# Kernel tuning notes

Hardware: AMD Instinct MI355X
Metric: run time of the kernel (lower is better)

The kernel has to match this reference:

```python
import jax, jax.numpy as jnp
import numpy as np

B, T, C, H = 4, 2048, 1024, 16
D = C // H  # head_dim = 64

def setup_inputs() -> dict:
    key = jax.random.key(0)
    ks = jax.random.split(key, 5)
    scale = 1.0 / np.sqrt(C)
    return {
        "x": jax.random.normal(ks[0], (B, T, C), dtype=jnp.float32),
        "Wq": jax.random.normal(ks[1], (C, C), dtype=jnp.float32) * scale,
        "Wk": jax.random.normal(ks[2], (C, C), dtype=jnp.float32) * scale,
        "Wv": jax.random.normal(ks[3], (C, C), dtype=jnp.float32) * scale,
        "Wo": jax.random.normal(ks[4], (C, C), dtype=jnp.float32) * scale,
        "bo": jnp.zeros((C,), dtype=jnp.float32),
    }

def reference(x, Wq, Wk, Wv, Wo, bo):
    Bx, Tx, Cx = x.shape
    # projections -> [B, H, T, D]
    def split_heads(y):
        return y.reshape(Bx, Tx, H, D).transpose(0, 2, 1, 3)
    Q = split_heads(x @ Wq)
    K = split_heads(x @ Wk)
    V = split_heads(x @ Wv)
    # scaled dot-product with causal mask: [B, H, T, T]
    scores = jnp.einsum('bhqd,bhkd->bhqk', Q, K) / jnp.sqrt(jnp.asarray(D, x.dtype))
    causal = jnp.tril(jnp.ones((Tx, Tx), dtype=bool))
    scores = jnp.where(causal, scores, -jnp.inf)
    weights = jax.nn.softmax(scores, axis=-1)
    attn = jnp.einsum('bhqk,bhkd->bhqd', weights, V)  # [B, H, T, D]
    out = attn.transpose(0, 2, 1, 3).reshape(Bx, Tx, Cx)
    return out @ Wo + bo
```

## Files before the change

### kernel.cpp

```cpp
#include <hip/hip_runtime.h>
#include <hip/hip_bf16.h>
#include <cmath>

typedef __bf16 bf16;
typedef __bf16 bf16x8 __attribute__((ext_vector_type(8)));
typedef __bf16 bf16x4v __attribute__((ext_vector_type(4)));
typedef float f32x4 __attribute__((ext_vector_type(4)));

#define B_ 4
#define T_ 2048
#define C_ 1024
#define H_ 16
#define D_ 64
#define BT_ 8192
#define LOG2E 1.4426950408889634f

__device__ __forceinline__ void async_cp16(const void* g, void* l) {
  __builtin_amdgcn_global_load_lds(
      (__attribute__((address_space(1))) void*)g,
      (__attribute__((address_space(3))) void*)l, 16, 0, 0);
}

__device__ __forceinline__ f32x4 mfma16(bf16x8 a, bf16x8 b, f32x4 c) {
  return __builtin_amdgcn_mfma_f32_16x16x32_bf16(a, b, c, 0, 0, 0);
}

__global__ __launch_bounds__(256) void cast_x_kernel(
    const float* __restrict__ in, bf16* __restrict__ out, int n4) {
  int i = blockIdx.x * 256 + threadIdx.x;
  if (i >= n4) return;
  float4 v = ((const float4*)in)[i];
  bf16x4v o = {(bf16)v.x, (bf16)v.y, (bf16)v.z, (bf16)v.w};
  ((bf16x4v*)out)[i] = o;
}

__global__ __launch_bounds__(256) void transpose_cast_kernel(
    const float* __restrict__ W, bf16* __restrict__ Wt) {
  __shared__ float tile[32][33];
  const int x = threadIdx.x, y = threadIdx.y;
  const int n0 = blockIdx.x * 32, k0 = blockIdx.y * 32;
#pragma unroll
  for (int j = 0; j < 32; j += 8)
    tile[y + j][x] = W[(size_t)(k0 + y + j) * C_ + n0 + x];
  __syncthreads();
#pragma unroll
  for (int j = 0; j < 32; j += 8)
    Wt[(size_t)(n0 + y + j) * C_ + k0 + x] = (bf16)tile[x][y + j];
}

template <int F32OUT>
__global__ __launch_bounds__(256, 2) void gemm_bt_kernel(
    const bf16* __restrict__ A, const bf16* __restrict__ Bt,
    void* __restrict__ Cv, const float* __restrict__ bias,
    int M, int N, int K) {
  __shared__ __align__(16) bf16 As[128 * 32];
  __shared__ __align__(16) bf16 Bs[128 * 32];
  const int t = threadIdx.x;
  const int lane = t & 63;
  const int wave = t >> 6;
  const int quad = lane >> 4;
  const int l15 = lane & 15;
  const int m0 = blockIdx.y * 128;
  const int n0 = blockIdx.x * 128;
  const int wm = (wave >> 1) * 64;
  const int wn = (wave & 1) * 64;
  const int srow = t >> 2;
  const int scol = (t & 3) * 8;

  const bf16* Ag = A + (size_t)(m0 + srow) * K + scol;
  const bf16* Bg = Bt + (size_t)(n0 + srow) * K + scol;
  bf16* Asd = &As[srow * 32 + scol];
  bf16* Asd2 = &As[(srow + 64) * 32 + scol];
  bf16* Bsd = &Bs[srow * 32 + scol];
  bf16* Bsd2 = &Bs[(srow + 64) * 32 + scol];

  f32x4 acc[4][4] = {};

  for (int kt = 0; kt < K; kt += 32) {
    async_cp16(Ag + kt, Asd);
    async_cp16(Ag + kt + (size_t)64 * K, Asd2);
    async_cp16(Bg + kt, Bsd);
    async_cp16(Bg + kt + (size_t)64 * K, Bsd2);
    __syncthreads();
    bf16x8 af[4], bfr[4];
#pragma unroll
    for (int i = 0; i < 4; i++)
      af[i] = *(const bf16x8*)&As[(wm + i * 16 + l15) * 32 + quad * 8];
#pragma unroll
    for (int j = 0; j < 4; j++)
      bfr[j] = *(const bf16x8*)&Bs[(wn + j * 16 + l15) * 32 + quad * 8];
#pragma unroll
    for (int i = 0; i < 4; i++)
#pragma unroll
      for (int j = 0; j < 4; j++)
        acc[i][j] = mfma16(af[i], bfr[j], acc[i][j]);
    __syncthreads();
  }

#pragma unroll
  for (int i = 0; i < 4; i++) {
    const int gr = m0 + wm + i * 16 + quad * 4;
#pragma unroll
    for (int j = 0; j < 4; j++) {
      const int gc = n0 + wn + j * 16 + l15;
      const float bv = F32OUT ? bias[gc] : 0.0f;
#pragma unroll
      for (int r = 0; r < 4; r++) {
        const float v = acc[i][j][r] + bv;
        if (F32OUT)
          ((float*)Cv)[(size_t)(gr + r) * N + gc] = v;
        else
          ((bf16*)Cv)[(size_t)(gr + r) * N + gc] = (bf16)v;
      }
    }
  }
}

__global__ __launch_bounds__(256, 3) void flash_attn_kernel(
    const bf16* __restrict__ qk, const bf16* __restrict__ vt,
    bf16* __restrict__ attn) {
  __shared__ __align__(16) char smem[49152];
  bf16* Ks = (bf16*)smem;
  bf16* Vs = (bf16*)(smem + 16384);
  bf16* Ps = (bf16*)(smem + 32768);

  const int t = threadIdx.x;
  const int lane = t & 63;
  const int wave = t >> 6;
  const int quad = lane >> 4;
  const int l15 = lane & 15;
  const int l7 = l15 & 7;
  const int bx = blockIdx.x;
  const int qt = 15 - (bx >> 6);
  const int bh = bx & 63;
  const int b = bh >> 4;
  const int h = bh & 15;

  const bf16* Qg = qk + (size_t)b * T_ * 2048 + h * 64;
  const bf16* Kg = qk + (size_t)b * T_ * 2048 + 1024 + h * 64;
  const bf16* Vg = vt + (size_t)h * 64 * BT_ + b * T_;

  bf16x8 qf[2][2];
  const int qrow0 = qt * 128 + wave * 32;
#pragma unroll
  for (int mt = 0; mt < 2; mt++)
#pragma unroll
    for (int ks = 0; ks < 2; ks++) {
      bf16x8 v = *(const bf16x8*)(Qg + (size_t)(qrow0 + mt * 16 + l15) * 2048 +
                                  ks * 32 + quad * 8);
#pragma unroll
      for (int j = 0; j < 8; j++) v[j] = (bf16)((float)v[j] * 0.125f);
      qf[mt][ks] = v;
    }

  f32x4 o_acc[4][2] = {};
  f32x4 l4[2] = {};

  const int krofs = lane >> 3;
  const int kck = (lane & 7) ^ krofs;
  const int vdofs = lane >> 4;
  const int vpc = lane & 15;
  const int pswz = (l15 & 3) << 2;

  for (int jt = 0; jt <= qt; jt++) {
    const int k0 = jt * 128;

    {
      const bf16* gK = Kg + (size_t)(k0 + wave * 32 + krofs) * 2048 + kck * 8;
      bf16* lK = Ks + wave * 2048 + lane * 8;
#pragma unroll
      for (int i = 0; i < 4; i++)
        async_cp16(gK + (size_t)(i * 8) * 2048, lK + i * 512);
    }
    {
#pragma unroll
      for (int i = 0; i < 4; i++) {
        const int d = wave * 16 + i * 4 + vdofs;
        const int cv = vpc ^ (d & 7);
        async_cp16(Vg + (size_t)d * BT_ + k0 + cv * 8,
                   Vs + (wave * 16 + i * 4) * 128 + lane * 8);
      }
    }
    __syncthreads();

    bf16x4v p[2][8];
    const bool diag = (jt == qt);
#pragma unroll
    for (int kt = 0; kt < 8; kt++) {
      const bf16x8 kf0 =
          *(const bf16x8*)&Ks[(kt * 16 + l15) * 64 + (quad ^ l7) * 8];
      const bf16x8 kf1 =
          *(const bf16x8*)&Ks[(kt * 16 + l15) * 64 + ((4 + quad) ^ l7) * 8];
#pragma unroll
      for (int mt = 0; mt < 2; mt++) {
        f32x4 s = mfma16(kf0, qf[mt][0], f32x4{0.f, 0.f, 0.f, 0.f});
        s = mfma16(kf1, qf[mt][1], s);
        if (diag) {
          const int q_loc = wave * 32 + mt * 16 + l15;
#pragma unroll
          for (int i = 0; i < 4; i++)
            if (kt * 16 + quad * 4 + i > q_loc) s[i] = -INFINITY;
        }
        f32x4 e;
#pragma unroll
        for (int i = 0; i < 4; i++)
          e[i] = __builtin_amdgcn_exp2f(s[i] * LOG2E);
        l4[mt] += e;
        p[mt][kt] = bf16x4v{(bf16)e[0], (bf16)e[1], (bf16)e[2], (bf16)e[3]};
      }
    }

#pragma unroll
    for (int hh = 0; hh < 2; hh++) {
#pragma unroll
      for (int mt = 0; mt < 2; mt++) {
        const int row = wave * 32 + mt * 16 + l15;
#pragma unroll
        for (int kt = 0; kt < 4; kt++) {
          const int c = kt * 4 + quad;
          *(bf16x4v*)&Ps[row * 64 + (c ^ pswz) * 4] = p[mt][hh * 4 + kt];
        }
      }
#pragma unroll
      for (int ks2 = 0; ks2 < 2; ks2++) {
        bf16x8 pa[2], vb[4];
#pragma unroll
        for (int mt = 0; mt < 2; mt++) {
          const int row = wave * 32 + mt * 16 + l15;
          const int c0 = ks2 * 8 + quad * 2;
          pa[mt] = *(const bf16x8*)&Ps[row * 64 + (c0 ^ pswz) * 4];
        }
#pragma unroll
        for (int dt = 0; dt < 4; dt++) {
          const int vc = (hh * 8 + ks2 * 4 + quad) ^ l7;
          vb[dt] = *(const bf16x8*)&Vs[(dt * 16 + l15) * 128 + vc * 8];
        }
#pragma unroll
        for (int dt = 0; dt < 4; dt++)
#pragma unroll
          for (int mt = 0; mt < 2; mt++)
            o_acc[dt][mt] = mfma16(vb[dt], pa[mt], o_acc[dt][mt]);
      }
    }
    __syncthreads();
  }

  float inv[2];
#pragma unroll
  for (int mt = 0; mt < 2; mt++) {
    float l = l4[mt][0] + l4[mt][1] + l4[mt][2] + l4[mt][3];
    l += __shfl_xor(l, 16, 64);
    l += __shfl_xor(l, 32, 64);
    inv[mt] = 1.0f / l;
  }
#pragma unroll
  for (int dt = 0; dt < 4; dt++)
#pragma unroll
    for (int mt = 0; mt < 2; mt++) {
      const int q = qt * 128 + wave * 32 + mt * 16 + l15;
      bf16x4v o = {(bf16)(o_acc[dt][mt][0] * inv[mt]),
                   (bf16)(o_acc[dt][mt][1] * inv[mt]),
                   (bf16)(o_acc[dt][mt][2] * inv[mt]),
                   (bf16)(o_acc[dt][mt][3] * inv[mt])};
      *(bf16x4v*)(attn + (size_t)(b * T_ + q) * 1024 + h * 64 + dt * 16 +
                  quad * 4) = o;
    }
}

extern "C" void kernel_launch(void* const* d_in, const int* in_sizes, int n_in,
                              void* d_out, int out_size, void* d_ws,
                              size_t ws_size, hipStream_t stream) {
  const float* x = (const float*)d_in[0];
  const float* Wq = (const float*)d_in[1];
  const float* Wk = (const float*)d_in[2];
  const float* Wv = (const float*)d_in[3];
  const float* Wo = (const float*)d_in[4];
  const float* bo = (const float*)d_in[5];
  float* out = (float*)d_out;

  char* ws = (char*)d_ws;
  bf16* xb = (bf16*)(ws);
  bf16* qkb = (bf16*)(ws + 16777216);
  bf16* vtb = (bf16*)(ws + 50331648);
  bf16* attn = (bf16*)(ws + 67108864);
  bf16* wqkvT = (bf16*)(ws + 83886080);
  bf16* woT = (bf16*)(ws + 90177536);

  cast_x_kernel<<<8192, 256, 0, stream>>>(x, xb, 2097152);

  dim3 tb(32, 8), tg(32, 32);
  transpose_cast_kernel<<<tg, tb, 0, stream>>>(Wq, wqkvT);
  transpose_cast_kernel<<<tg, tb, 0, stream>>>(Wk, wqkvT + 1024 * 1024);
  transpose_cast_kernel<<<tg, tb, 0, stream>>>(Wv, wqkvT + 2 * 1024 * 1024);
  transpose_cast_kernel<<<tg, tb, 0, stream>>>(Wo, woT);

  gemm_bt_kernel<0><<<dim3(16, 64), 256, 0, stream>>>(
      xb, wqkvT, (void*)qkb, nullptr, 8192, 2048, 1024);

  gemm_bt_kernel<0><<<dim3(64, 8), 256, 0, stream>>>(
      wqkvT + 2 * 1024 * 1024, xb, (void*)vtb, nullptr, 1024, 8192, 1024);

  flash_attn_kernel<<<1024, 256, 0, stream>>>(qkb, vtb, attn);

  gemm_bt_kernel<1><<<dim3(8, 64), 256, 0, stream>>>(
      attn, woT, (void*)out, bo, 8192, 1024, 1024);
}
```

Baseline: 270.9 us.

## Double-buffer attention KV tiles, widen GEMM K-tile, merge weight transposes

The flash attention loop now works on 64-key tiles with two LDS buffers, issuing the async load of the next tile before computing the current one. This is meant to hide global-load latency and removes the trailing barrier. The GEMM now uses a 64-wide K tile with an XOR-swizzled LDS layout and occupancy hint 3, halving barrier count per K. The four weight transpose-cast launches are merged into one 3D-grid launch. Risks: more LDS per block could limit occupancy, and smaller attention tiles double the number of barriers per key range.

New measurement: 239.8 us. 11.5% less time.

```diff
diff --git a/kernel.cpp b/kernel.cpp
--- a/kernel.cpp
+++ b/kernel.cpp
@@ -34,9 +34,14 @@
   ((bf16x4v*)out)[i] = o;
 }
 
-__global__ __launch_bounds__(256) void transpose_cast_kernel(
-    const float* __restrict__ W, bf16* __restrict__ Wt) {
+__global__ __launch_bounds__(256) void transpose_cast4_kernel(
+    const float* __restrict__ Wq, const float* __restrict__ Wk,
+    const float* __restrict__ Wv, const float* __restrict__ Wo,
+    bf16* __restrict__ dst) {
   __shared__ float tile[32][33];
+  const int z = blockIdx.z;
+  const float* W = (z == 0) ? Wq : (z == 1) ? Wk : (z == 2) ? Wv : Wo;
+  bf16* Wt = dst + (size_t)z * 1048576;
   const int x = threadIdx.x, y = threadIdx.y;
   const int n0 = blockIdx.x * 32, k0 = blockIdx.y * 32;
 #pragma unroll
@@ -49,51 +54,56 @@
 }
 
 template <int F32OUT>
-__global__ __launch_bounds__(256, 2) void gemm_bt_kernel(
+__global__ __launch_bounds__(256, 3) void gemm_bt_kernel(
     const bf16* __restrict__ A, const bf16* __restrict__ Bt,
     void* __restrict__ Cv, const float* __restrict__ bias,
     int M, int N, int K) {
-  __shared__ __align__(16) bf16 As[128 * 32];
-  __shared__ __align__(16) bf16 Bs[128 * 32];
+  __shared__ __align__(16) bf16 As[128 * 64];
+  __shared__ __align__(16) bf16 Bs[128 * 64];
   const int t = threadIdx.x;
   const int lane = t & 63;
   const int wave = t >> 6;
   const int quad = lane >> 4;
   const int l15 = lane & 15;
+  const int l7 = l15 & 7;
   const int m0 = blockIdx.y * 128;
   const int n0 = blockIdx.x * 128;
   const int wm = (wave >> 1) * 64;
   const int wn = (wave & 1) * 64;
-  const int srow = t >> 2;
-  const int scol = (t & 3) * 8;
-
-  const bf16* Ag = A + (size_t)(m0 + srow) * K + scol;
-  const bf16* Bg = Bt + (size_t)(n0 + srow) * K + scol;
-  bf16* Asd = &As[srow * 32 + scol];
-  bf16* Asd2 = &As[(srow + 64) * 32 + scol];
-  bf16* Bsd = &Bs[srow * 32 + scol];
-  bf16* Bsd2 = &Bs[(srow + 64) * 32 + scol];
+
+  const int sr8 = lane >> 3;
+  const int sc = (lane & 7) ^ sr8;
+  const bf16* Ag = A + (size_t)(m0 + wave * 32 + sr8) * K + sc * 8;
+  const bf16* Bg = Bt + (size_t)(n0 + wave * 32 + sr8) * K + sc * 8;
+  bf16* Ad = As + wave * 2048 + lane * 8;
+  bf16* Bd = Bs + wave * 2048 + lane * 8;
 
   f32x4 acc[4][4] = {};
 
-  for (int kt = 0; kt < K; kt += 32) {
-    async_cp16(Ag + kt, Asd);
-    async_cp16(Ag + kt + (size_t)64 * K, Asd2);
-    async_cp16(Bg + kt, Bsd);
-    async_cp16(Bg + kt + (size_t)64 * K, Bsd2);
+  for (int kt = 0; kt < K; kt += 64) {
+#pragma unroll
+    for (int i = 0; i < 4; i++) {
+      async_cp16(Ag + kt + (size_t)(i * 8) * K, Ad + i * 512);
+      async_cp16(Bg + kt + (size_t)(i * 8) * K, Bd + i * 512);
+    }
     __syncthreads();
-    bf16x8 af[4], bfr[4];
-#pragma unroll
-    for (int i = 0; i < 4; i++)
-      af[i] = *(const bf16x8*)&As[(wm + i * 16 + l15) * 32 + quad * 8];
-#pragma unroll
-    for (int j = 0; j < 4; j++)
-      bfr[j] = *(const bf16x8*)&Bs[(wn + j * 16 + l15) * 32 + quad * 8];
-#pragma unroll
-    for (int i = 0; i < 4; i++)
+#pragma unroll
+    for (int ks = 0; ks < 2; ks++) {
+      bf16x8 af[4], bfr[4];
+#pragma unroll
+      for (int i = 0; i < 4; i++)
+        af[i] = *(const bf16x8*)&As[(wm + i * 16 + l15) * 64 +
+                                    (((ks * 4 + quad) ^ l7) * 8)];
 #pragma unroll
       for (int j = 0; j < 4; j++)
-        acc[i][j] = mfma16(af[i], bfr[j], acc[i][j]);
+        bfr[j] = *(const bf16x8*)&Bs[(wn + j * 16 + l15) * 64 +
+                                     (((ks * 4 + quad) ^ l7) * 8)];
+#pragma unroll
+      for (int i = 0; i < 4; i++)
+#pragma unroll
+        for (int j = 0; j < 4; j++)
+          acc[i][j] = mfma16(af[i], bfr[j], acc[i][j]);
+    }
     __syncthreads();
   }
 
@@ -119,9 +129,9 @@
 __global__ __launch_bounds__(256, 3) void flash_attn_kernel(
     const bf16* __restrict__ qk, const bf16* __restrict__ vt,
     bf16* __restrict__ attn) {
-  __shared__ __align__(16) char smem[49152];
-  bf16* Ks = (bf16*)smem;
-  bf16* Vs = (bf16*)(smem + 16384);
+  __shared__ __align__(16) char smem[51200];
+  bf16* KsB = (bf16*)smem;
+  bf16* VsB = (bf16*)(smem + 16384);
   bf16* Ps = (bf16*)(smem + 32768);
 
   const int t = threadIdx.x;
@@ -156,93 +166,83 @@
   f32x4 o_acc[4][2] = {};
   f32x4 l4[2] = {};
 
-  const int krofs = lane >> 3;
-  const int kck = (lane & 7) ^ krofs;
-  const int vdofs = lane >> 4;
-  const int vpc = lane & 15;
-  const int pswz = (l15 & 3) << 2;
-
-  for (int jt = 0; jt <= qt; jt++) {
-    const int k0 = jt * 128;
-
-    {
-      const bf16* gK = Kg + (size_t)(k0 + wave * 32 + krofs) * 2048 + kck * 8;
-      bf16* lK = Ks + wave * 2048 + lane * 8;
-#pragma unroll
-      for (int i = 0; i < 4; i++)
-        async_cp16(gK + (size_t)(i * 8) * 2048, lK + i * 512);
-    }
-    {
-#pragma unroll
-      for (int i = 0; i < 4; i++) {
-        const int d = wave * 16 + i * 4 + vdofs;
-        const int cv = vpc ^ (d & 7);
-        async_cp16(Vg + (size_t)d * BT_ + k0 + cv * 8,
-                   Vs + (wave * 16 + i * 4) * 128 + lane * 8);
-      }
-    }
+  const int sr8 = lane >> 3;
+  const int sc = (lane & 7) ^ sr8;
+
+  auto stage = [&](int j64, int buf) {
+    const int k0 = j64 * 64;
+    bf16* KL = KsB + buf * 4096 + wave * 1024 + lane * 8;
+    const bf16* KG = Kg + (size_t)(k0 + wave * 16 + sr8) * 2048 + sc * 8;
+    async_cp16(KG, KL);
+    async_cp16(KG + (size_t)8 * 2048, KL + 512);
+    bf16* VL = VsB + buf * 4096 + wave * 1024 + lane * 8;
+    const bf16* VG = Vg + (size_t)(wave * 16 + sr8) * BT_ + k0 + sc * 8;
+    async_cp16(VG, VL);
+    async_cp16(VG + (size_t)8 * BT_, VL + 512);
+  };
+
+  const int S = 2 * qt + 2;
+  stage(0, 0);
+
+  for (int s = 0; s < S; s++) {
     __syncthreads();
-
-    bf16x4v p[2][8];
-    const bool diag = (jt == qt);
-#pragma unroll
-    for (int kt = 0; kt < 8; kt++) {
+    if (s + 1 < S) stage(s + 1, (s + 1) & 1);
+    const bf16* Kb = KsB + (s & 1) * 4096;
+    const bf16* Vb = VsB + (s & 1) * 4096;
+    const int k0 = s * 64;
+    const bool diag = (s >= 2 * qt);
+
+    bf16x4v p[2][4];
+#pragma unroll
+    for (int kt = 0; kt < 4; kt++) {
       const bf16x8 kf0 =
-          *(const bf16x8*)&Ks[(kt * 16 + l15) * 64 + (quad ^ l7) * 8];
+          *(const bf16x8*)&Kb[(kt * 16 + l15) * 64 + ((quad ^ l7) * 8)];
       const bf16x8 kf1 =
-          *(const bf16x8*)&Ks[(kt * 16 + l15) * 64 + ((4 + quad) ^ l7) * 8];
+          *(const bf16x8*)&Kb[(kt * 16 + l15) * 64 + (((4 + quad) ^ l7) * 8)];
 #pragma unroll
       for (int mt = 0; mt < 2; mt++) {
-        f32x4 s = mfma16(kf0, qf[mt][0], f32x4{0.f, 0.f, 0.f, 0.f});
-        s = mfma16(kf1, qf[mt][1], s);
+        f32x4 sv = mfma16(kf0, qf[mt][0], f32x4{0.f, 0.f, 0.f, 0.f});
+        sv = mfma16(kf1, qf[mt][1], sv);
         if (diag) {
-          const int q_loc = wave * 32 + mt * 16 + l15;
+          const int qg = qt * 128 + wave * 32 + mt * 16 + l15;
 #pragma unroll
           for (int i = 0; i < 4; i++)
-            if (kt * 16 + quad * 4 + i > q_loc) s[i] = -INFINITY;
+            if (k0 + kt * 16 + quad * 4 + i > qg) sv[i] = -INFINITY;
         }
         f32x4 e;
 #pragma unroll
         for (int i = 0; i < 4; i++)
-          e[i] = __builtin_amdgcn_exp2f(s[i] * LOG2E);
+          e[i] = __builtin_amdgcn_exp2f(sv[i] * LOG2E);
         l4[mt] += e;
         p[mt][kt] = bf16x4v{(bf16)e[0], (bf16)e[1], (bf16)e[2], (bf16)e[3]};
       }
     }
 
 #pragma unroll
-    for (int hh = 0; hh < 2; hh++) {
-#pragma unroll
-      for (int mt = 0; mt < 2; mt++) {
-        const int row = wave * 32 + mt * 16 + l15;
-#pragma unroll
-        for (int kt = 0; kt < 4; kt++) {
-          const int c = kt * 4 + quad;
-          *(bf16x4v*)&Ps[row * 64 + (c ^ pswz) * 4] = p[mt][hh * 4 + kt];
-        }
-      }
-#pragma unroll
-      for (int ks2 = 0; ks2 < 2; ks2++) {
-        bf16x8 pa[2], vb[4];
-#pragma unroll
-        for (int mt = 0; mt < 2; mt++) {
-          const int row = wave * 32 + mt * 16 + l15;
-          const int c0 = ks2 * 8 + quad * 2;
-          pa[mt] = *(const bf16x8*)&Ps[row * 64 + (c0 ^ pswz) * 4];
-        }
-#pragma unroll
-        for (int dt = 0; dt < 4; dt++) {
-          const int vc = (hh * 8 + ks2 * 4 + quad) ^ l7;
-          vb[dt] = *(const bf16x8*)&Vs[(dt * 16 + l15) * 128 + vc * 8];
-        }
-#pragma unroll
-        for (int dt = 0; dt < 4; dt++)
-#pragma unroll
-          for (int mt = 0; mt < 2; mt++)
-            o_acc[dt][mt] = mfma16(vb[dt], pa[mt], o_acc[dt][mt]);
-      }
-    }
-    __syncthreads();
+    for (int mt = 0; mt < 2; mt++) {
+      const int row = wave * 32 + mt * 16 + l15;
+#pragma unroll
+      for (int kt = 0; kt < 4; kt++)
+        *(bf16x4v*)&Ps[row * 72 + kt * 16 + quad * 4] = p[mt][kt];
+    }
+
+#pragma unroll
+    for (int ks2 = 0; ks2 < 2; ks2++) {
+      bf16x8 pa[2], vb[4];
+#pragma unroll
+      for (int mt = 0; mt < 2; mt++)
+        pa[mt] = *(const bf16x8*)&Ps[(wave * 32 + mt * 16 + l15) * 72 +
+                                     ks2 * 32 + quad * 8];
+#pragma unroll
+      for (int dt = 0; dt < 4; dt++)
+        vb[dt] = *(const bf16x8*)&Vb[(dt * 16 + l15) * 64 +
+                                     (((ks2 * 4 + quad) ^ l7) * 8)];
+#pragma unroll
+      for (int dt = 0; dt < 4; dt++)
+#pragma unroll
+        for (int mt = 0; mt < 2; mt++)
+          o_acc[dt][mt] = mfma16(vb[dt], pa[mt], o_acc[dt][mt]);
+    }
   }
 
   float inv[2];
@@ -288,11 +288,8 @@
 
   cast_x_kernel<<<8192, 256, 0, stream>>>(x, xb, 2097152);
 
-  dim3 tb(32, 8), tg(32, 32);
-  transpose_cast_kernel<<<tg, tb, 0, stream>>>(Wq, wqkvT);
-  transpose_cast_kernel<<<tg, tb, 0, stream>>>(Wk, wqkvT + 1024 * 1024);
-  transpose_cast_kernel<<<tg, tb, 0, stream>>>(Wv, wqkvT + 2 * 1024 * 1024);
-  transpose_cast_kernel<<<tg, tb, 0, stream>>>(Wo, woT);
+  transpose_cast4_kernel<<<dim3(32, 32, 4), dim3(32, 8), 0, stream>>>(
+      Wq, Wk, Wv, Wo, wqkvT);
 
   gemm_bt_kernel<0><<<dim3(16, 64), 256, 0, stream>>>(
       xb, wqkvT, (void*)qkb, nullptr, 8192, 2048, 1024);
```
